# Kernel tuning notes

Hardware: AMD Instinct MI355X
Metric: run time of the kernel (lower is better)

## Reference

```python
import jax, jax.numpy as jnp
import numpy as np
from jax import lax

D_MODEL = 1024
D_STATE = 16
D_CONV = 4
D_INNER = 2 * D_MODEL
B_SZ = 2
L_SEQ = 1024
EPS = 1e-5


def setup_inputs() -> dict:
    key = jax.random.key(0)
    ks = jax.random.split(key, 8)
    s = lambda k, shape, scale: jax.random.normal(k, shape, jnp.float32) * scale
    return {
        "x": jax.random.normal(ks[0], (B_SZ, L_SEQ, D_MODEL), jnp.float32),
        "norm_w": jnp.ones((D_MODEL,), jnp.float32),
        "norm_b": jnp.zeros((D_MODEL,), jnp.float32),
        "in_proj_w": s(ks[1], (2 * D_INNER, D_MODEL), 0.02),
        "in_proj_b": jnp.zeros((2 * D_INNER,), jnp.float32),
        "conv_w": s(ks[2], (D_INNER, 1, D_CONV), 0.1),   # torch Conv1d weight (out, in/groups, k)
        "conv_b": jnp.zeros((D_INNER,), jnp.float32),
        "x_proj_w": s(ks[3], (2 * D_STATE, D_INNER), 0.02),
        "x_proj_b": jnp.zeros((2 * D_STATE,), jnp.float32),
        "dt_proj_w": s(ks[4], (D_INNER, D_INNER), 0.02),
        "dt_proj_b": jnp.zeros((D_INNER,), jnp.float32),
        "A_log": s(ks[5], (D_INNER, D_STATE), 1.0),
        "D_param": jnp.ones((D_INNER,), jnp.float32),
        "out_proj_w": s(ks[6], (D_MODEL, D_INNER), 0.02),
        "out_proj_b": jnp.zeros((D_MODEL,), jnp.float32),
    }


def _layernorm(x, w, b):
    mu = jnp.mean(x, axis=-1, keepdims=True)
    var = jnp.mean(jnp.square(x - mu), axis=-1, keepdims=True)
    return (x - mu) * lax.rsqrt(var + EPS) * w + b


def _silu(x):
    return x * jax.nn.sigmoid(x)


def _selective_scan(u, delta, A, B_ssm, C_ssm):
    # u, delta: (B, L, d_inner); A: (d_inner, d_state); B_ssm, C_ssm: (B, L, d_state)
    dA = jnp.exp(delta[..., None] * A)                    # (B, L, d_inner, d_state)
    dBu = (delta * u)[..., None] * B_ssm[:, :, None, :]   # (B, L, d_inner, d_state)
    # time-major for scan
    dA_t = jnp.moveaxis(dA, 1, 0)
    dBu_t = jnp.moveaxis(dBu, 1, 0)
    C_t = jnp.moveaxis(C_ssm, 1, 0)

    def step(h, inp):
        dA_i, dBu_i, c_i = inp
        h = dA_i * h + dBu_i                              # (B, d_inner, d_state)
        y = jnp.einsum('bds,bs->bd', h, c_i)
        return h, y

    h0 = jnp.zeros((u.shape[0], u.shape[2], A.shape[1]), u.dtype)
    _, ys = lax.scan(step, h0, (dA_t, dBu_t, C_t))
    return jnp.moveaxis(ys, 0, 1)                         # (B, L, d_inner)


def reference(x, norm_w, norm_b, in_proj_w, in_proj_b, conv_w, conv_b,
              x_proj_w, x_proj_b, dt_proj_w, dt_proj_b, A_log, D_param,
              out_proj_w, out_proj_b):
    residual = x
    xn = _layernorm(x, norm_w, norm_b)
    xz = xn @ in_proj_w.T + in_proj_b                     # (B, L, 2*d_inner)
    xc, z = jnp.split(xz, 2, axis=-1)
    # depthwise causal conv1d (torch pads both sides d_conv-1 then slices :L == left pad)
    kern = jnp.transpose(conv_w, (2, 1, 0))               # (k, 1, d_inner) for 'LIO'
    xc = lax.conv_general_dilated(
        xc, kern, window_strides=(1,), padding=[(D_CONV - 1, 0)],
        dimension_numbers=('NLC', 'LIO', 'NLC'), feature_group_count=D_INNER) + conv_b
    u = _silu(xc)
    x_db = u @ x_proj_w.T + x_proj_b                      # (B, L, 2*d_state)
    B_ssm, C_ssm = jnp.split(x_db, 2, axis=-1)
    delta = jax.nn.softplus(u @ dt_proj_w.T + dt_proj_b)  # (B, L, d_inner)
    A = -jnp.exp(A_log)
    y = _selective_scan(u, delta, A, B_ssm, C_ssm)
    y = y + u * D_param
    y = y * _silu(z)
    out = y @ out_proj_w.T + out_proj_b
    return residual + out
```

## Files before the change

kernel.cpp:

```cpp
#include <hip/hip_runtime.h>

#define DM   1024
#define DI   2048
#define LSEQ 1024
#define BSZ  2
#define MROWS (BSZ*LSEQ)
#define NCH   (BSZ*DI)
#define SCHUNK 32
#define STEPS  32
#define PLANE  (NCH*16)

typedef __attribute__((ext_vector_type(4)))  float  f32x4;
typedef __attribute__((ext_vector_type(8)))  __bf16 bf16x8;

__device__ __forceinline__ unsigned short f2bf(float f) {
  union { float f; unsigned int u; } v; v.f = f;
  unsigned int u = v.u;
  unsigned int r = (u + 0x7fffu + ((u >> 16) & 1u)) >> 16;
  return (unsigned short)r;
}

__device__ __forceinline__ void load_lds16(const void* g, void* l) {
  __builtin_amdgcn_global_load_lds((const __attribute__((address_space(1))) void*)g,
                                   (__attribute__((address_space(3))) void*)l, 16, 0, 0);
}

__global__ __launch_bounds__(256) void ln_cast(const float* __restrict__ x,
    const float* __restrict__ w, const float* __restrict__ b,
    unsigned short* __restrict__ out)
{
  int row = blockIdx.x, tid = threadIdx.x;
  const float4* xr = (const float4*)(x + (size_t)row * DM);
  float4 v = xr[tid];
  float s  = v.x + v.y + v.z + v.w;
  float s2 = v.x*v.x + v.y*v.y + v.z*v.z + v.w*v.w;
  #pragma unroll
  for (int off = 32; off > 0; off >>= 1) { s += __shfl_down(s, off); s2 += __shfl_down(s2, off); }
  __shared__ float ss[4], sq[4];
  if ((tid & 63) == 0) { ss[tid >> 6] = s; sq[tid >> 6] = s2; }
  __syncthreads();
  float mean = (ss[0]+ss[1]+ss[2]+ss[3]) * (1.0f/DM);
  float var  = (sq[0]+sq[1]+sq[2]+sq[3]) * (1.0f/DM) - mean*mean;
  float rs = rsqrtf(var + 1e-5f);
  float4 wv = ((const float4*)w)[tid];
  float4 bv = ((const float4*)b)[tid];
  ushort4 o;
  o.x = f2bf((v.x-mean)*rs*wv.x + bv.x);
  o.y = f2bf((v.y-mean)*rs*wv.y + bv.y);
  o.z = f2bf((v.z-mean)*rs*wv.z + bv.z);
  o.w = f2bf((v.w-mean)*rs*wv.w + bv.w);
  ((ushort4*)(out + (size_t)row * DM))[tid] = o;
}

__global__ __launch_bounds__(256) void castk(const float* __restrict__ in,
    unsigned short* __restrict__ out, int n4)
{
  int i = blockIdx.x * 256 + threadIdx.x;
  int stride = gridDim.x * 256;
  for (; i < n4; i += stride) {
    float4 v = ((const float4*)in)[i];
    ushort4 o;
    o.x = f2bf(v.x); o.y = f2bf(v.y); o.z = f2bf(v.z); o.w = f2bf(v.w);
    ((ushort4*)out)[i] = o;
  }
}

template<int EPI>
__global__ __launch_bounds__(256) void gemm_bt(
    const unsigned short* __restrict__ A, const unsigned short* __restrict__ Bw,
    const float* __restrict__ bias, const float* __restrict__ resid,
    float* __restrict__ C, int N, int K)
{
  __shared__ unsigned short As[2][128*64];
  __shared__ unsigned short Bs[2][64*64];
  const int tid  = threadIdx.x;
  const int lane = tid & 63;
  const int w    = tid >> 6;

  const int nbx = gridDim.x;
  const int nwg = gridDim.x * gridDim.y;
  int wg  = blockIdx.y * nbx + blockIdx.x;
  int swz = (wg & 7) * (nwg >> 3) + (wg >> 3);
  const int m0 = (swz / nbx) * 128;
  const int n0 = (swz % nbx) * 64;

  const int wm = w >> 1, wn = w & 1;
  const int r16 = lane & 15;
  const int kg  = lane >> 4;

  const int srow = tid >> 3;
  const int kl   = (tid & 7) ^ (srow & 7);
  const unsigned short* gaBase = A  + (size_t)(m0 + srow) * K + kl * 8;
  const unsigned short* gbBase = Bw + (size_t)(n0 + srow) * K + kl * 8;

  f32x4 acc[4][2] = {};

  auto stage = [&](int buf, int kt) {
    const unsigned short* ga = gaBase + kt;
    load_lds16(ga,                   (char*)As[buf] + tid*16);
    load_lds16(ga + (size_t)32*K,    (char*)As[buf] +  4096 + tid*16);
    load_lds16(ga + (size_t)64*K,    (char*)As[buf] +  8192 + tid*16);
    load_lds16(ga + (size_t)96*K,    (char*)As[buf] + 12288 + tid*16);
    const unsigned short* gb = gbBase + kt;
    load_lds16(gb,                   (char*)Bs[buf] + tid*16);
    load_lds16(gb + (size_t)32*K,    (char*)Bs[buf] +  4096 + tid*16);
  };

  stage(0, 0);
  stage(1, 64);

  int cur = 0;
  for (int kt = 0; kt < K; kt += 64) {
    if (kt + 64 < K) asm volatile("s_waitcnt vmcnt(6)" ::: "memory");
    else             asm volatile("s_waitcnt vmcnt(0)" ::: "memory");
    __builtin_amdgcn_s_barrier();

    bf16x8 av[2][4], bv[2][2];
    #pragma unroll
    for (int kk = 0; kk < 2; ++kk) {
      const int phys = (kk*4 + kg) ^ (r16 & 7);
      #pragma unroll
      for (int i = 0; i < 4; ++i)
        av[kk][i] = *(const bf16x8*)((const char*)As[cur] + (wm*64 + i*16 + r16)*128 + phys*16);
      #pragma unroll
      for (int j = 0; j < 2; ++j)
        bv[kk][j] = *(const bf16x8*)((const char*)Bs[cur] + (wn*32 + j*16 + r16)*128 + phys*16);
    }
    #pragma unroll
    for (int kk = 0; kk < 2; ++kk)
      #pragma unroll
      for (int i = 0; i < 4; ++i)
        #pragma unroll
        for (int j = 0; j < 2; ++j)
          acc[i][j] = __builtin_amdgcn_mfma_f32_16x16x32_bf16(av[kk][i], bv[kk][j], acc[i][j], 0, 0, 0);

    asm volatile("s_waitcnt lgkmcnt(0)" ::: "memory");
    __builtin_amdgcn_s_barrier();
    if (kt + 128 < K) stage(cur, kt + 128);
    cur ^= 1;
  }

  #pragma unroll
  for (int i = 0; i < 4; ++i) {
    int rbase = m0 + wm*64 + i*16 + kg*4;
    #pragma unroll
    for (int j = 0; j < 2; ++j) {
      int col = n0 + wn*32 + j*16 + r16;
      float bcol = bias[col];
      #pragma unroll
      for (int r = 0; r < 4; ++r) {
        int row = rbase + r;
        float v = acc[i][j][r] + bcol;
        if (EPI == 1) v = (v > 20.f) ? v : log1pf(__expf(v));
        if (EPI == 2) v += resid[(size_t)row * N + col];
        C[(size_t)row * N + col] = v;
      }
    }
  }
}

__global__ __launch_bounds__(256) void conv_silu(const float* __restrict__ xz,
    const float* __restrict__ cw, const float* __restrict__ cb,
    float* __restrict__ u, unsigned short* __restrict__ u_bf)
{
  int idx = blockIdx.x * 256 + threadIdx.x;
  int d = idx & (DI-1);
  int m = idx >> 11;
  int l = m & (LSEQ-1);
  const float* col = xz + (size_t)m * (2*DI) + d;
  float acc = cb[d];
  float w0 = cw[d*4+0], w1 = cw[d*4+1], w2 = cw[d*4+2], w3 = cw[d*4+3];
  acc += w3 * col[0];
  if (l >= 1) acc += w2 * col[-(2*DI)];
  if (l >= 2) acc += w1 * col[-2*(2*DI)];
  if (l >= 3) acc += w0 * col[-3*(2*DI)];
  float s = acc / (1.f + __expf(-acc));
  u[idx]    = s;
  u_bf[idx] = f2bf(s);
}

__global__ __launch_bounds__(64) void xproj_mfma(const unsigned short* __restrict__ u_bf,
    const unsigned short* __restrict__ wx, const float* __restrict__ bias,
    float* __restrict__ xdb)
{
  int lane = threadIdx.x;
  int m0 = blockIdx.x * 16;
  int r16 = lane & 15, kg = lane >> 4;
  f32x4 acc0 = {}, acc1 = {};
  const unsigned short* ap  = u_bf + (size_t)(m0 + r16) * DI + kg*8;
  const unsigned short* b0p = wx   + (size_t)r16        * DI + kg*8;
  const unsigned short* b1p = wx   + (size_t)(16 + r16) * DI + kg*8;
  #pragma unroll 4
  for (int kt = 0; kt < DI; kt += 32) {
    bf16x8 a  = *(const bf16x8*)(ap  + kt);
    bf16x8 b0 = *(const bf16x8*)(b0p + kt);
    bf16x8 b1 = *(const bf16x8*)(b1p + kt);
    acc0 = __builtin_amdgcn_mfma_f32_16x16x32_bf16(a, b0, acc0, 0, 0, 0);
    acc1 = __builtin_amdgcn_mfma_f32_16x16x32_bf16(a, b1, acc1, 0, 0, 0);
  }
  #pragma unroll
  for (int r = 0; r < 4; ++r) {
    int row = m0 + kg*4 + r;
    xdb[row*32 + r16]      = acc0[r] + bias[r16];
    xdb[row*32 + 16 + r16] = acc1[r] + bias[16 + r16];
  }
}

__global__ __launch_bounds__(256) void scan_p1(const float* __restrict__ delta,
    const float* __restrict__ u, const float* __restrict__ xdb,
    const float* __restrict__ A_log, float* __restrict__ agg_a, float* __restrict__ agg_b)
{
  int tid = threadIdx.x;
  int sh  = tid & 3;
  int ch  = blockIdx.x * 64 + (tid >> 2);
  int c   = blockIdx.y;
  int b = ch >> 11, d = ch & (DI-1);
  float Ads[4];
  {
    f32x4 Ar = *(const f32x4*)(A_log + d*16 + sh*4);
    #pragma unroll
    for (int s = 0; s < 4; ++s) Ads[s] = -__expf(Ar[s]);
  }
  float a[4] = {1.f,1.f,1.f,1.f}, bb[4] = {0.f,0.f,0.f,0.f};
  int row0 = b * LSEQ + c * STEPS;
  const float* dp = delta + (size_t)row0 * DI + d;
  const float* up = u     + (size_t)row0 * DI + d;
  #pragma unroll 4
  for (int t = 0; t < STEPS; ++t) {
    float dl = dp[t*DI];
    float uu = up[t*DI];
    f32x4 Bv = *(const f32x4*)(xdb + (size_t)(row0 + t) * 32 + sh*4);
    float dlu = dl * uu;
    #pragma unroll
    for (int s = 0; s < 4; ++s) {
      float dA = __expf(dl * Ads[s]);
      bb[s] = fmaf(dA, bb[s], dlu * Bv[s]);
      a[s] *= dA;
    }
  }
  int idx = c*PLANE + ch*16 + sh*4;
  f32x4 av, bv;
  #pragma unroll
  for (int s = 0; s < 4; ++s) { av[s] = a[s]; bv[s] = bb[s]; }
  *(f32x4*)(agg_a + idx) = av;
  *(f32x4*)(agg_b + idx) = bv;
}

__global__ __launch_bounds__(256) void scan_p2(const float* __restrict__ agg_a,
    const float* __restrict__ agg_b, float* __restrict__ hinit)
{
  int idx = blockIdx.x * 256 + threadIdx.x;
  float h = 0.f;
  #pragma unroll
  for (int c = 0; c < SCHUNK; ++c) {
    hinit[c*PLANE + idx] = h;
    h = fmaf(agg_a[c*PLANE + idx], h, agg_b[c*PLANE + idx]);
  }
}

__global__ __launch_bounds__(256) void scan_p3(const float* __restrict__ delta,
    const float* __restrict__ u, const float* __restrict__ xdb,
    const float* __restrict__ A_log, const float* __restrict__ Dp,
    const float* __restrict__ xz, const float* __restrict__ hinit,
    unsigned short* __restrict__ y_bf)
{
  int tid = threadIdx.x;
  int sh  = tid & 3;
  int ch  = blockIdx.x * 64 + (tid >> 2);
  int c   = blockIdx.y;
  int b = ch >> 11, d = ch & (DI-1);
  float Ads[4];
  {
    f32x4 Ar = *(const f32x4*)(A_log + d*16 + sh*4);
    #pragma unroll
    for (int s = 0; s < 4; ++s) Ads[s] = -__expf(Ar[s]);
  }
  float h[4];
  {
    f32x4 hv = *(const f32x4*)(hinit + c*PLANE + ch*16 + sh*4);
    #pragma unroll
    for (int s = 0; s < 4; ++s) h[s] = hv[s];
  }
  float Dd = Dp[d];
  int row0 = b * LSEQ + c * STEPS;
  const float* dp = delta + (size_t)row0 * DI + d;
  const float* up = u     + (size_t)row0 * DI + d;
  const float* zp = xz    + (size_t)row0 * (2*DI) + DI + d;
  unsigned short* yp = y_bf + (size_t)row0 * DI + d;
  #pragma unroll 2
  for (int t = 0; t < STEPS; ++t) {
    float dl = dp[t*DI];
    float uu = up[t*DI];
    const float* xr = xdb + (size_t)(row0 + t) * 32 + sh*4;
    f32x4 Bv = *(const f32x4*)xr;
    f32x4 Cv = *(const f32x4*)(xr + 16);
    float dlu = dl * uu;
    float y = 0.f;
    #pragma unroll
    for (int s = 0; s < 4; ++s) {
      float dA = __expf(dl * Ads[s]);
      h[s] = fmaf(dA, h[s], dlu * Bv[s]);
      y = fmaf(h[s], Cv[s], y);
    }
    y += __shfl_xor(y, 1);
    y += __shfl_xor(y, 2);
    if (sh == 0) {
      float zz = zp[t*(2*DI)];
      float yv = y + uu * Dd;
      yv *= zz / (1.f + __expf(-zz));
      yp[t*DI] = f2bf(yv);
    }
  }
}

extern "C" void kernel_launch(void* const* d_in, const int* in_sizes, int n_in,
                              void* d_out, int out_size, void* d_ws, size_t ws_size,
                              hipStream_t stream)
{
  (void)in_sizes; (void)n_in; (void)out_size;
  const float* x      = (const float*)d_in[0];
  const float* norm_w = (const float*)d_in[1];
  const float* norm_b = (const float*)d_in[2];
  const float* in_w   = (const float*)d_in[3];
  const float* in_b   = (const float*)d_in[4];
  const float* conv_w = (const float*)d_in[5];
  const float* conv_b = (const float*)d_in[6];
  const float* xp_w   = (const float*)d_in[7];
  const float* xp_b   = (const float*)d_in[8];
  const float* dt_w   = (const float*)d_in[9];
  const float* dt_b   = (const float*)d_in[10];
  const float* A_log  = (const float*)d_in[11];
  const float* D_par  = (const float*)d_in[12];
  const float* out_w  = (const float*)d_in[13];
  const float* out_b  = (const float*)d_in[14];
  float* out = (float*)d_out;

  char* p = (char*)d_ws;
  unsigned short* xn_bf = (unsigned short*)p;  p += 2048ull*1024*2;
  unsigned short* w_in  = (unsigned short*)p;  p += 4096ull*1024*2;
  unsigned short* w_dt  = (unsigned short*)p;  p += 2048ull*2048*2;
  unsigned short* w_out = (unsigned short*)p;  p += 1024ull*2048*2;
  unsigned short* wx_bf = (unsigned short*)p;  p += 32ull*2048*2;
  float*          xz    = (float*)p;           p += 2048ull*4096*4;
  float*          u_f   = (float*)p;           p += 2048ull*2048*4;
  unsigned short* u_bf  = (unsigned short*)p;  p += 2048ull*2048*2;
  float*          xdb   = (float*)p;           p += 2048ull*32*4;
  float*          delta = (float*)p;           p += 2048ull*2048*4;
  unsigned short* y_bf  = (unsigned short*)p;  p += 2048ull*2048*2;
  if ((size_t)(p - (char*)d_ws) > ws_size) return;

  float* agg_a = (float*)w_in;
  float* agg_b = (float*)w_dt;
  float* hinit = (float*)u_bf;

  ln_cast<<<MROWS, 256, 0, stream>>>(x, norm_w, norm_b, xn_bf);
  castk<<<2048, 256, 0, stream>>>(in_w,  w_in,  4096*1024/4);
  castk<<<2048, 256, 0, stream>>>(dt_w,  w_dt,  2048*2048/4);
  castk<<<1024, 256, 0, stream>>>(out_w, w_out, 1024*2048/4);
  castk<<<64,   256, 0, stream>>>(xp_w,  wx_bf, 32*2048/4);

  gemm_bt<0><<<dim3(4096/64, MROWS/128), 256, 0, stream>>>(xn_bf, w_in, in_b, nullptr, xz, 4096, 1024);
  conv_silu<<<(MROWS*DI)/256, 256, 0, stream>>>(xz, conv_w, conv_b, u_f, u_bf);
  xproj_mfma<<<MROWS/16, 64, 0, stream>>>(u_bf, wx_bf, xp_b, xdb);
  gemm_bt<1><<<dim3(2048/64, MROWS/128), 256, 0, stream>>>(u_bf, w_dt, dt_b, nullptr, delta, 2048, 2048);

  scan_p1<<<dim3(NCH/64, SCHUNK), 256, 0, stream>>>(delta, u_f, xdb, A_log, agg_a, agg_b);
  scan_p2<<<PLANE/256, 256, 0, stream>>>(agg_a, agg_b, hinit);
  scan_p3<<<dim3(NCH/64, SCHUNK), 256, 0, stream>>>(delta, u_f, xdb, A_log, D_par, xz, hinit, y_bf);

  gemm_bt<2><<<dim3(1024/64, MROWS/128), 256, 0, stream>>>(y_bf, w_out, out_b, x, out, 1024, 2048);
}
```

Baseline: 221.8 us.

## Store intermediate activations in bf16 and merge weight-cast launches

The in_proj output (xz) and the dt_proj/softplus output (delta) are now written as bf16 instead of fp32. The fp32 copy of u is dropped, and conv and the scan kernels read bf16 and widen it in registers. This roughly halves memory traffic for the largest intermediates between the GEMMs, conv and scan. The four weight-cast launches are also merged into one kernel, and hinit moves to its own buffer because u_bf can no longer be aliased. The cost is lower precision for delta, u and z inside the scan, which may affect accuracy.

Measured after the change: 211.5 us. 4.6% less time.

```diff
diff --git a/kernel.cpp b/kernel.cpp
--- a/kernel.cpp
+++ b/kernel.cpp
@@ -18,6 +18,9 @@
   unsigned int u = v.u;
   unsigned int r = (u + 0x7fffu + ((u >> 16) & 1u)) >> 16;
   return (unsigned short)r;
+}
+__device__ __forceinline__ float bf2f(unsigned short h) {
+  union { unsigned int u; float f; } v; v.u = (unsigned int)h << 16; return v.f;
 }
 
 __device__ __forceinline__ void load_lds16(const void* g, void* l) {
@@ -52,24 +55,34 @@
   ((ushort4*)(out + (size_t)row * DM))[tid] = o;
 }
 
-__global__ __launch_bounds__(256) void castk(const float* __restrict__ in,
-    unsigned short* __restrict__ out, int n4)
-{
+__global__ __launch_bounds__(256) void cast_all(
+    const float* __restrict__ s0, unsigned short* __restrict__ d0,
+    const float* __restrict__ s1, unsigned short* __restrict__ d1,
+    const float* __restrict__ s2, unsigned short* __restrict__ d2,
+    const float* __restrict__ s3, unsigned short* __restrict__ d3)
+{
+  const int N0 = 4096*1024/4, N1 = 2048*2048/4, N2 = 1024*2048/4, N3 = 32*2048/4;
   int i = blockIdx.x * 256 + threadIdx.x;
   int stride = gridDim.x * 256;
-  for (; i < n4; i += stride) {
-    float4 v = ((const float4*)in)[i];
+  int total = N0 + N1 + N2 + N3;
+  for (; i < total; i += stride) {
+    const float* s; unsigned short* d; int j = i;
+    if (j < N0) { s = s0; d = d0; }
+    else if ((j -= N0) < N1) { s = s1; d = d1; }
+    else if ((j -= N1) < N2) { s = s2; d = d2; }
+    else { j -= N2; s = s3; d = d3; }
+    float4 v = ((const float4*)s)[j];
     ushort4 o;
     o.x = f2bf(v.x); o.y = f2bf(v.y); o.z = f2bf(v.z); o.w = f2bf(v.w);
-    ((ushort4*)out)[i] = o;
-  }
-}
-
-template<int EPI>
+    ((ushort4*)d)[j] = o;
+  }
+}
+
+template<int EPI, typename OT>
 __global__ __launch_bounds__(256) void gemm_bt(
     const unsigned short* __restrict__ A, const unsigned short* __restrict__ Bw,
     const float* __restrict__ bias, const float* __restrict__ resid,
-    float* __restrict__ C, int N, int K)
+    OT* __restrict__ C, int N, int K)
 {
   __shared__ unsigned short As[2][128*64];
   __shared__ unsigned short Bs[2][64*64];
@@ -153,29 +166,29 @@
         float v = acc[i][j][r] + bcol;
         if (EPI == 1) v = (v > 20.f) ? v : log1pf(__expf(v));
         if (EPI == 2) v += resid[(size_t)row * N + col];
-        C[(size_t)row * N + col] = v;
+        if constexpr (sizeof(OT) == 2) C[(size_t)row * N + col] = f2bf(v);
+        else                           C[(size_t)row * N + col] = v;
       }
     }
   }
 }
 
-__global__ __launch_bounds__(256) void conv_silu(const float* __restrict__ xz,
+__global__ __launch_bounds__(256) void conv_silu(const unsigned short* __restrict__ xz,
     const float* __restrict__ cw, const float* __restrict__ cb,
-    float* __restrict__ u, unsigned short* __restrict__ u_bf)
+    unsigned short* __restrict__ u_bf)
 {
   int idx = blockIdx.x * 256 + threadIdx.x;
   int d = idx & (DI-1);
   int m = idx >> 11;
   int l = m & (LSEQ-1);
-  const float* col = xz + (size_t)m * (2*DI) + d;
+  const unsigned short* col = xz + (size_t)m * (2*DI) + d;
   float acc = cb[d];
   float w0 = cw[d*4+0], w1 = cw[d*4+1], w2 = cw[d*4+2], w3 = cw[d*4+3];
-  acc += w3 * col[0];
-  if (l >= 1) acc += w2 * col[-(2*DI)];
-  if (l >= 2) acc += w1 * col[-2*(2*DI)];
-  if (l >= 3) acc += w0 * col[-3*(2*DI)];
+  acc += w3 * bf2f(col[0]);
+  if (l >= 1) acc += w2 * bf2f(col[-(2*DI)]);
+  if (l >= 2) acc += w1 * bf2f(col[-2*(2*DI)]);
+  if (l >= 3) acc += w0 * bf2f(col[-3*(2*DI)]);
   float s = acc / (1.f + __expf(-acc));
-  u[idx]    = s;
   u_bf[idx] = f2bf(s);
 }
 
@@ -206,8 +219,8 @@
   }
 }
 
-__global__ __launch_bounds__(256) void scan_p1(const float* __restrict__ delta,
-    const float* __restrict__ u, const float* __restrict__ xdb,
+__global__ __launch_bounds__(256) void scan_p1(const unsigned short* __restrict__ delta,
+    const unsigned short* __restrict__ u, const float* __restrict__ xdb,
     const float* __restrict__ A_log, float* __restrict__ agg_a, float* __restrict__ agg_b)
 {
   int tid = threadIdx.x;
@@ -223,12 +236,12 @@
   }
   float a[4] = {1.f,1.f,1.f,1.f}, bb[4] = {0.f,0.f,0.f,0.f};
   int row0 = b * LSEQ + c * STEPS;
-  const float* dp = delta + (size_t)row0 * DI + d;
-  const float* up = u     + (size_t)row0 * DI + d;
+  const unsigned short* dp = delta + (size_t)row0 * DI + d;
+  const unsigned short* up = u     + (size_t)row0 * DI + d;
   #pragma unroll 4
   for (int t = 0; t < STEPS; ++t) {
-    float dl = dp[t*DI];
-    float uu = up[t*DI];
+    float dl = bf2f(dp[t*DI]);
+    float uu = bf2f(up[t*DI]);
     f32x4 Bv = *(const f32x4*)(xdb + (size_t)(row0 + t) * 32 + sh*4);
     float dlu = dl * uu;
     #pragma unroll
@@ -258,10 +271,10 @@
   }
 }
 
-__global__ __launch_bounds__(256) void scan_p3(const float* __restrict__ delta,
-    const float* __restrict__ u, const float* __restrict__ xdb,
+__global__ __launch_bounds__(256) void scan_p3(const unsigned short* __restrict__ delta,
+    const unsigned short* __restrict__ u, const float* __restrict__ xdb,
     const float* __restrict__ A_log, const float* __restrict__ Dp,
-    const float* __restrict__ xz, const float* __restrict__ hinit,
+    const unsigned short* __restrict__ xz, const float* __restrict__ hinit,
     unsigned short* __restrict__ y_bf)
 {
   int tid = threadIdx.x;
@@ -283,14 +296,14 @@
   }
   float Dd = Dp[d];
   int row0 = b * LSEQ + c * STEPS;
-  const float* dp = delta + (size_t)row0 * DI + d;
-  const float* up = u     + (size_t)row0 * DI + d;
-  const float* zp = xz    + (size_t)row0 * (2*DI) + DI + d;
+  const unsigned short* dp = delta + (size_t)row0 * DI + d;
+  const unsigned short* up = u     + (size_t)row0 * DI + d;
+  const unsigned short* zp = xz    + (size_t)row0 * (2*DI) + DI + d;
   unsigned short* yp = y_bf + (size_t)row0 * DI + d;
   #pragma unroll 2
   for (int t = 0; t < STEPS; ++t) {
-    float dl = dp[t*DI];
-    float uu = up[t*DI];
+    float dl = bf2f(dp[t*DI]);
+    float uu = bf2f(up[t*DI]);
     const float* xr = xdb + (size_t)(row0 + t) * 32 + sh*4;
     f32x4 Bv = *(const f32x4*)xr;
     f32x4 Cv = *(const f32x4*)(xr + 16);
@@ -305,7 +318,7 @@
     y += __shfl_xor(y, 1);
     y += __shfl_xor(y, 2);
     if (sh == 0) {
-      float zz = zp[t*(2*DI)];
+      float zz = bf2f(zp[t*(2*DI)]);
       float yv = y + uu * Dd;
       yv *= zz / (1.f + __expf(-zz));
       yp[t*DI] = f2bf(yv);
@@ -341,32 +354,28 @@
   unsigned short* w_dt  = (unsigned short*)p;  p += 2048ull*2048*2;
   unsigned short* w_out = (unsigned short*)p;  p += 1024ull*2048*2;
   unsigned short* wx_bf = (unsigned short*)p;  p += 32ull*2048*2;
-  float*          xz    = (float*)p;           p += 2048ull*4096*4;
-  float*          u_f   = (float*)p;           p += 2048ull*2048*4;
+  unsigned short* xz    = (unsigned short*)p;  p += 2048ull*4096*2;
   unsigned short* u_bf  = (unsigned short*)p;  p += 2048ull*2048*2;
   float*          xdb   = (float*)p;           p += 2048ull*32*4;
-  float*          delta = (float*)p;           p += 2048ull*2048*4;
+  unsigned short* delta = (unsigned short*)p;  p += 2048ull*2048*2;
   unsigned short* y_bf  = (unsigned short*)p;  p += 2048ull*2048*2;
+  float*          hinit = (float*)p;           p += (size_t)PLANE*SCHUNK*4;
   if ((size_t)(p - (char*)d_ws) > ws_size) return;
 
   float* agg_a = (float*)w_in;
   float* agg_b = (float*)w_dt;
-  float* hinit = (float*)u_bf;
-
+
+  cast_all<<<2048, 256, 0, stream>>>(in_w, w_in, dt_w, w_dt, out_w, w_out, xp_w, wx_bf);
   ln_cast<<<MROWS, 256, 0, stream>>>(x, norm_w, norm_b, xn_bf);
-  castk<<<2048, 256, 0, stream>>>(in_w,  w_in,  4096*1024/4);
-  castk<<<2048, 256, 0, stream>>>(dt_w,  w_dt,  2048*2048/4);
-  castk<<<1024, 256, 0, stream>>>(out_w, w_out, 1024*2048/4);
-  castk<<<64,   256, 0, stream>>>(xp_w,  wx_bf, 32*2048/4);
-
-  gemm_bt<0><<<dim3(4096/64, MROWS/128), 256, 0, stream>>>(xn_bf, w_in, in_b, nullptr, xz, 4096, 1024);
-  conv_silu<<<(MROWS*DI)/256, 256, 0, stream>>>(xz, conv_w, conv_b, u_f, u_bf);
+
+  gemm_bt<0, unsigned short><<<dim3(4096/64, MROWS/128), 256, 0, stream>>>(xn_bf, w_in, in_b, nullptr, xz, 4096, 1024);
+  conv_silu<<<(MROWS*DI)/256, 256, 0, stream>>>(xz, conv_w, conv_b, u_bf);
   xproj_mfma<<<MROWS/16, 64, 0, stream>>>(u_bf, wx_bf, xp_b, xdb);
-  gemm_bt<1><<<dim3(2048/64, MROWS/128), 256, 0, stream>>>(u_bf, w_dt, dt_b, nullptr, delta, 2048, 2048);
-
-  scan_p1<<<dim3(NCH/64, SCHUNK), 256, 0, stream>>>(delta, u_f, xdb, A_log, agg_a, agg_b);
+  gemm_bt<1, unsigned short><<<dim3(2048/64, MROWS/128), 256, 0, stream>>>(u_bf, w_dt, dt_b, nullptr, delta, 2048, 2048);
+
+  scan_p1<<<dim3(NCH/64, SCHUNK), 256, 0, stream>>>(delta, u_bf, xdb, A_log, agg_a, agg_b);
   scan_p2<<<PLANE/256, 256, 0, stream>>>(agg_a, agg_b, hinit);
-  scan_p3<<<dim3(NCH/64, SCHUNK), 256, 0, stream>>>(delta, u_f, xdb, A_log, D_par, xz, hinit, y_bf);
-
-  gemm_bt<2><<<dim3(1024/64, MROWS/128), 256, 0, stream>>>(y_bf, w_out, out_b, x, out, 1024, 2048);
-}
+  scan_p3<<<dim3(NCH/64, SCHUNK), 256, 0, stream>>>(delta, u_bf, xdb, A_log, D_par, xz, hinit, y_bf);
+
+  gemm_bt<2, float><<<dim3(1024/64, MROWS/128), 256, 0, stream>>>(y_bf, w_out, out_b, x, out, 1024, 2048);
+}
```
